# Kernel optimization log

Hardware: AMD Instinct MI355X
Metric: run time of the kernel (lower is better)

Reference implementation:

```python
import jax, jax.numpy as jnp
import numpy as np

NB, NC, IN, HID, OUT, ENG = 8, 16384, 64, 128, 64, 128
SYNC, DEBATE = 0.15, 0.15


def setup_inputs() -> dict:
    key = jax.random.key(0)
    ks = jax.random.split(key, 24)
    rn = lambda k, s, sc=0.05: jax.random.normal(k, s, jnp.float32) * sc
    return {
        "x": jax.random.normal(ks[0], (1, IN), jnp.float32),
        "noise": jax.random.normal(ks[1], (NB, 1, IN), jnp.float32),
        "amps": jax.random.uniform(ks[2], (NB,), jnp.float32, 0.5, 1.5),
        "hiddens": jax.random.normal(ks[3], (NB, NC, HID), jnp.float32) * 0.1,
        "eaW1": rn(ks[4], (ENG, IN + HID)), "eaB1": rn(ks[5], (ENG,)),
        "eaW2": rn(ks[6], (OUT, ENG)), "eaB2": rn(ks[7], (OUT,)),
        "egW1": rn(ks[8], (ENG, IN + HID)), "egB1": rn(ks[9], (ENG,)),
        "egW2": rn(ks[10], (OUT, ENG)), "egB2": rn(ks[11], (OUT,)),
        "gru_Wih": rn(ks[12], (3 * HID, OUT + 1)), "gru_Whh": rn(ks[13], (3 * HID, HID)),
        "gru_bih": rn(ks[14], (3 * HID,)), "gru_bhh": rn(ks[15], (3 * HID,)),
        "headW": rn(ks[16], (IN, OUT)), "headb": rn(ks[17], (IN,)),
        "mixW": rn(ks[18], (HID, HID * NB)), "mixb": rn(ks[19], (HID,)),
        "step": 10,
    }


def reference(x, noise, amps, hiddens, eaW1, eaB1, eaW2, eaB2,
              egW1, egB1, egW2, egB2, gru_Wih, gru_Whh, gru_bih, gru_bhh,
              headW, headb, mixW, mixb, step):
    sg = jax.lax.stop_gradient
    # per-branch perturbed input, broadcast over cells
    scale = 0.05 * jnp.arange(1, NB + 1, dtype=x.dtype)[:, None, None]
    xb = jnp.broadcast_to(x[None] + noise * scale, (NB, NC, IN))
    comb = jnp.concatenate([xb, hiddens], axis=-1)          # (NB,NC,IN+HID)
    a = jax.nn.relu(comb @ eaW1.T + eaB1) @ eaW2.T + eaB2
    g = jax.nn.relu(comb @ egW1.T + egB1) @ egW2.T + egB2
    out = a - g                                             # (NB,NC,OUT)
    tension = jnp.mean(out ** 2, axis=-1)                   # (NB,NC)

    # GRUCell update (mem input is detached in the original)
    mem_in = sg(jnp.concatenate([out, tension[..., None]], axis=-1))
    gi = mem_in @ gru_Wih.T + gru_bih                       # (NB,NC,3H)
    gh = hiddens @ gru_Whh.T + gru_bhh
    ir, iz, inn = jnp.split(gi, 3, axis=-1)
    hr, hz, hn = jnp.split(gh, 3, axis=-1)
    r = jax.nn.sigmoid(ir + hr)
    z = jax.nn.sigmoid(iz + hz)
    n = jnp.tanh(inn + r * hn)
    newh = sg((1.0 - z) * n + z * hiddens)                  # stored detached

    # faction sync + debate (state only)
    nf = min(8, NC // 2)
    fs = NC // nf
    core = newh[:, :nf * fs].reshape(NB, nf, fs, HID)
    core = (1.0 - SYNC) * core + SYNC * core.mean(axis=2, keepdims=True)
    if step > 5:
        glob = core.mean(axis=2).mean(axis=1)               # (NB,HID)
        dc = max(1, fs // 4)
        core = core.at[:, :, :dc].set(
            (1.0 - DEBATE) * core[:, :, :dc] + DEBATE * glob[:, None, None, :])
    newh = jnp.concatenate([core.reshape(NB, nf * fs, HID), newh[:, nf * fs:]], axis=1)

    # amplitude-weighted branch combine (amps used via .item() -> constants)
    aabs = jnp.abs(amps)
    aabs = aabs / (aabs.sum() + 1e-8)
    cell_out = jnp.einsum('b,bnd->nd', sg(aabs), out)       # (NC,OUT)
    avg_t = tension.mean(axis=0)                            # (NC,)
    w = jax.nn.softmax(sg(avg_t))                           # weights from .item()'d tensions
    combined = (w[:, None] * cell_out).sum(axis=0, keepdims=True)  # (1,OUT)
    pred = combined @ headW.T + headb                       # (1,IN)

    # interference mixer state update on branch 0
    interf = newh.mean(axis=1).reshape(1, -1) @ mixW.T + mixb       # (1,HID)
    newh = newh.at[0].add(sg(interf) * 0.05)

    return pred, avg_t.mean(), newh
```

## Files before the change

### kernel.cpp

```cpp
#include <hip/hip_runtime.h>
#include <math.h>

#define NB   8
#define NCC  16384
#define HID  128

typedef __attribute__((ext_vector_type(8))) short short8;
typedef __attribute__((ext_vector_type(4))) float f32x4;

#define MFMA(a,b,c) __builtin_amdgcn_mfma_f32_16x16x32_bf16(a,b,c,0,0,0)

#define WS_AABS   0
#define WS_BASE1  8
#define WS_BOUT   2056
#define WS_BSUMR  2120
#define WS_BSUMZ  2248
#define WS_BIHN   2376
#define WS_BHHN   2504
#define WS_W64    2632
#define WS_INTERF 3024
#define WS_FRAG   3152
#define WS_SD     64592
#define WS_AVGT   73808
#define WS_TS     90192
#define WS_FMEAN  221264
#define WS_PART2  230480
#define WS_FPART  246864
#define WS_CO     771152
#define WS_PARTE  1819728
#define WS_PARTA  1819984

__device__ __forceinline__ unsigned short f2b(float f) {
    unsigned int u = __float_as_uint(f);
    unsigned int r = (u + 0x7fffu + ((u >> 16) & 1u)) >> 16;
    return (unsigned short)r;
}
__device__ __forceinline__ float b2f(unsigned short us) {
    return __uint_as_float(((unsigned int)us) << 16);
}
__device__ __forceinline__ float sigm(float x) {
    return __builtin_amdgcn_rcpf(1.f + __expf(-x));
}
__device__ __forceinline__ float tanh_fast(float x) {
    return 1.f - 2.f * __builtin_amdgcn_rcpf(__expf(2.f * x) + 1.f);
}
__device__ __forceinline__ unsigned int cvtpk(float lo, float hi) {
    unsigned int r;
    asm volatile("v_cvt_pk_bf16_f32 %0, %1, %2" : "=v"(r) : "v"(lo), "v"(hi));
    return r;
}
__device__ __forceinline__ void stg(char* dst, int row, int cb, float4 u, float4 v) {
    uint4 pk = make_uint4(cvtpk(u.x, u.y), cvtpk(u.z, u.w),
                          cvtpk(v.x, v.y), cvtpk(v.z, v.w));
    *(uint4*)(dst + row * 256 + (cb ^ ((row & 7) << 4))) = pk;
}

__global__ __launch_bounds__(1024) void kprep(
    const float* __restrict__ x, const float* __restrict__ noise,
    const float* __restrict__ amps,
    const float* __restrict__ eaW1, const float* __restrict__ eaB1,
    const float* __restrict__ egW1, const float* __restrict__ egB1,
    const float* __restrict__ eaW2, const float* __restrict__ eaB2,
    const float* __restrict__ egW2, const float* __restrict__ egB2,
    const float* __restrict__ gWih, const float* __restrict__ gWhh,
    const float* __restrict__ gbih, const float* __restrict__ gbhh,
    float* __restrict__ ws)
{
    int i = blockIdx.x * 1024 + threadIdx.x;
    if (i < 122880) {
        short* wsh = (short*)(ws + WS_FRAG);
        float v;
        if (i < 32768) {
            int rel = i;
            int j = rel & 7, l = (rel >> 3) & 63, tk = rel >> 9;
            int kt = tk & 3, nt = tk >> 2;
            int n = nt * 16 + (l & 15), k = kt * 32 + ((l >> 4) << 3) + j;
            v = (n < 128) ? eaW1[n * 192 + 64 + k] : egW1[(n - 128) * 192 + 64 + k];
        } else if (i < 49152) {
            int rel = i - 32768;
            int j = rel & 7, l = (rel >> 3) & 63, tk = rel >> 9;
            int kt = tk & 7, nt = tk >> 3;
            int d = nt * 16 + (l & 15), k = kt * 32 + ((l >> 4) << 3) + j;
            v = (k < 128) ? eaW2[d * 128 + k] : -egW2[d * 128 + (k - 128)];
        } else if (i < 73728) {
            int rel = i - 49152;
            int j = rel & 7, l = (rel >> 3) & 63, tk = rel >> 9;
            int kt = tk & 1, nt = tk >> 1;
            int r = nt * 16 + (l & 15), k = kt * 32 + ((l >> 4) << 3) + j;
            v = gWih[r * 65 + k];
        } else {
            int rel = i - 73728;
            int j = rel & 7, l = (rel >> 3) & 63, tk = rel >> 9;
            int kt = tk & 3, nt = tk >> 2;
            int r = nt * 16 + (l & 15), k = kt * 32 + ((l >> 4) << 3) + j;
            v = gWhh[r * 128 + k];
        }
        wsh[i] = (short)f2b(v);
    }
    if (blockIdx.x == 0) {
        __shared__ float xb[8][64];
        int t = threadIdx.x;
        if (t < 512) {
            int b = t >> 6, k = t & 63;
            xb[b][k] = x[k] + noise[b * 64 + k] * (0.05f * (float)(b + 1));
        }
        if (t == 0) {
            float s = 0.f;
            for (int b = 0; b < 8; b++) s += fabsf(amps[b]);
            s += 1e-8f;
            for (int b = 0; b < 8; b++) ws[WS_AABS + b] = fabsf(amps[b]) / s;
        }
        __syncthreads();
        for (int ii = t; ii < 2048; ii += 1024) {
            int b = ii >> 8, n = ii & 255;
            const float* Wp; float s;
            if (n < 128) { Wp = eaW1 + n * 192; s = eaB1[n]; }
            else         { Wp = egW1 + (n - 128) * 192; s = egB1[n - 128]; }
            for (int k = 0; k < 64; k++) s += xb[b & 7][k] * Wp[k];
            ws[WS_BASE1 + ii] = s;
        }
        if (t < 64) ws[WS_BOUT + t] = eaB2[t] - egB2[t];
        if (t < 128) {
            ws[WS_BSUMR + t] = gbih[t] + gbhh[t];
            ws[WS_BSUMZ + t] = gbih[128 + t] + gbhh[128 + t];
            ws[WS_BIHN + t]  = gbih[256 + t];
            ws[WS_BHHN + t]  = gbhh[256 + t];
        }
        if (t < 384) ws[WS_W64 + t] = gWih[t * 65 + 64];
    }
}

__global__ __launch_bounds__(1024) void kA(
    const float* __restrict__ hiddens, float* __restrict__ newh,
    float* __restrict__ ws)
{
    __shared__ char  wlds[98304];
    __shared__ char  hsb[64 * 256];
    __shared__ char  agb[64 * 512];
    __shared__ float ts_s[64];
    __shared__ float tsum_s[64];

    const int t    = threadIdx.x;
    const int lane = t & 63;
    const int w    = t >> 6;
    const int rg   = w >> 2;
    const int nq   = w & 3;
    const int col  = lane & 15;
    const int kq   = lane >> 4;
    const int r0   = rg * 16;
    const int n0   = blockIdx.x * 64;

    {
        const float4* src = (const float4*)(ws + WS_FRAG);
        float4* dst = (float4*)wlds;
#pragma unroll
        for (int p = 0; p < 6; p++) dst[p * 1024 + t] = src[p * 1024 + t];
    }
    const short8* W1F = (const short8*)wlds;
    const short8* W2F = (const short8*)(wlds + 65536);

    const float bo = ws[WS_BOUT + nq * 16 + col];
    float co_reg[4];
#pragma unroll
    for (int i = 0; i < 4; i++) co_reg[i] = 0.f;
    if (t < 64) tsum_s[t] = 0.f;

    const int flat = t * 8;
    const int srow = flat >> 7;
    const int scb  = (flat & 127) * 2;

    {
        const float* hs = hiddens + (size_t)n0 * HID;
        float4 a0 = *(const float4*)(hs + flat);
        float4 a1 = *(const float4*)(hs + flat + 4);
        stg(hsb, srow, scb, a0, a1);
    }
    float4 pfa0, pfa1;
    unsigned short* outu = (unsigned short*)newh;

    for (int b = 0; b < NB; ++b) {
        __syncthreads();
        if (t < 64) {
            if (b > 0) {
                ws[WS_TS + (size_t)(b - 1) * NCC + n0 + t] = ts_s[t];
                tsum_s[t] += ts_s[t];
            }
            ts_s[t] = 0.f;
        }
        if (b < 7) {
            const float* hsn = hiddens + ((size_t)((b + 1) * NCC + n0)) * HID;
            pfa0 = *(const float4*)(hsn + flat);
            pfa1 = *(const float4*)(hsn + flat + 4);
        }

        {
            short8 aH[4];
#pragma unroll
            for (int ks = 0; ks < 4; ks++) {
                int row = r0 + col;
                aH[ks] = *(const short8*)(hsb + row * 256 +
                           ((ks * 64 + (kq << 4)) ^ ((row & 7) << 4)));
            }
#pragma unroll
            for (int nti = 0; nti < 4; nti++) {
                int nt = nq * 4 + nti;
                f32x4 ac = {0.f, 0.f, 0.f, 0.f};
#pragma unroll
                for (int kt = 0; kt < 4; kt++)
                    ac = MFMA(aH[kt], W1F[(nt * 4 + kt) * 64 + lane], ac);
                int n = nt * 16 + col;
                float bs = ws[WS_BASE1 + b * 256 + n];
#pragma unroll
                for (int j = 0; j < 4; j++) {
                    int row = r0 + (kq << 2) + j;
                    float v = fmaxf(ac[j] + bs, 0.f);
                    *(unsigned short*)(agb + row * 512 +
                        ((n * 2) ^ ((row & 7) << 4))) = f2b(v);
                }
            }
        }
        __syncthreads();

        if (b < 7) stg(hsb, srow, scb, pfa0, pfa1);

        {
            f32x4 ov = {0.f, 0.f, 0.f, 0.f};
#pragma unroll
            for (int kt = 0; kt < 8; kt++) {
                int kb = kt * 64 + (kq << 4);
                int ra = r0 + col;
                short8 a0 = *(const short8*)(agb + ra * 512 + (kb ^ ((ra & 7) << 4)));
                ov = MFMA(a0, W2F[(nq * 8 + kt) * 64 + lane], ov);
            }
            int d = nq * 16 + col;
            float aab = ws[WS_AABS + b];
#pragma unroll
            for (int j = 0; j < 4; j++) {
                int row = r0 + (kq << 2) + j;
                float v = ov[j] + bo;
                co_reg[j] += aab * v;
                outu[(size_t)(b * NCC + n0 + row) * 256 + 192 + d] = f2b(v);
                float sq = v * v;
                sq += __shfl_xor(sq, 1);
                sq += __shfl_xor(sq, 2);
                sq += __shfl_xor(sq, 4);
                sq += __shfl_xor(sq, 8);
                if (col == 0) atomicAdd(&ts_s[row], sq);
            }
        }
    }
    __syncthreads();
    if (t < 64) {
        ws[WS_TS + (size_t)7 * NCC + n0 + t] = ts_s[t];
        tsum_s[t] += ts_s[t];
        ws[WS_AVGT + n0 + t] = tsum_s[t] * (1.f / 512.f);
    }
    {
        int d = nq * 16 + col;
#pragma unroll
        for (int j = 0; j < 4; j++) {
            int row = r0 + (kq << 2) + j;
            ws[WS_CO + (size_t)(n0 + row) * 64 + d] = co_reg[j];
        }
    }
}

__global__ __launch_bounds__(1024) void kB(
    const float* __restrict__ hiddens, float* __restrict__ newh,
    float* __restrict__ ws)
{
    __shared__ char  wl[98304];
    __shared__ char  hsb[64 * 256];
    __shared__ char  otb[64 * 128];
    __shared__ float ts_s[64];
    __shared__ float fp2[2][128];

    const int t    = threadIdx.x;
    const int lane = t & 63;
    const int w    = t >> 6;
    const int rg   = w >> 3;
    const int hg   = w & 7;
    const int col  = lane & 15;
    const int kq   = lane >> 4;
    const int chunk = blockIdx.x;
    const int n0   = chunk * 64;

    {
        const float4* src = (const float4*)(ws + WS_FRAG) + 9216;
        float4* dst = (float4*)wl;
#pragma unroll
        for (int p = 0; p < 6; p++) dst[p * 1024 + t] = src[p * 1024 + t];
    }
    const short8* WHHF = (const short8*)wl;
    const unsigned short* outu = (const unsigned short*)newh;

    const short8* WIHG = (const short8*)((const short*)(ws + WS_FRAG) + 49152);
    short8 wihR[2], wihZ[2], wihI[2];
#pragma unroll
    for (int ks = 0; ks < 2; ks++) {
        wihR[ks] = WIHG[(hg * 2 + ks) * 64 + lane];
        wihZ[ks] = WIHG[((hg + 8) * 2 + ks) * 64 + lane];
        wihI[ks] = WIHG[((hg + 16) * 2 + ks) * 64 + lane];
    }

    const int h = hg * 16 + col;
    const float bsr = ws[WS_BSUMR + h];
    const float bsz = ws[WS_BSUMZ + h];
    const float bin = ws[WS_BIHN + h];
    const float bhn = ws[WS_BHHN + h];
    const float wr  = ws[WS_W64 + h];
    const float wz  = ws[WS_W64 + 128 + h];
    const float wn  = ws[WS_W64 + 256 + h];

    const int flat = t * 8;
    const int srow = flat >> 7;
    const int scb  = (flat & 127) * 2;
    const int ocell = t >> 4;
    const int ooff  = (t & 15) * 4;

    float4 rh0, rh1;
    uint2  ro;
    float  rts = 0.f;
    {
        const float* hs = hiddens + (size_t)n0 * HID;
        rh0 = *(const float4*)(hs + flat);
        rh1 = *(const float4*)(hs + flat + 4);
        ro  = *(const uint2*)(outu + (size_t)(n0 + ocell) * 256 + 192 + ooff);
    }
    if (t < 64) rts = ws[WS_TS + n0 + t];

    for (int b = 0; b < NB; ++b) {
        stg(hsb, srow, scb, rh0, rh1);
        *(uint2*)(otb + ocell * 128 + ((ooff * 2) ^ ((ocell & 7) << 4))) = ro;
        if (t < 64) ts_s[t] = rts;
        __syncthreads();

        if (b < 7) {
            const float* hsn = hiddens + ((size_t)((b + 1) * NCC + n0)) * HID;
            rh0 = *(const float4*)(hsn + flat);
            rh1 = *(const float4*)(hsn + flat + 4);
            ro  = *(const uint2*)(outu + (size_t)((b + 1) * NCC + n0 + ocell) * 256 + 192 + ooff);
            if (t < 64) rts = ws[WS_TS + (size_t)(b + 1) * NCC + n0 + t];
        }

        {
            float* nbase = newh + ((size_t)(b * NCC + n0)) * HID;
            float flsum = 0.f;
#pragma unroll
            for (int st = 0; st < 2; ++st) {
                const int rbase = rg * 32 + st * 16;
                const int ra = rbase + col;
                f32x4 R = {0.f,0.f,0.f,0.f};
                f32x4 Z = {0.f,0.f,0.f,0.f};
                f32x4 I = {0.f,0.f,0.f,0.f};
                f32x4 N = {0.f,0.f,0.f,0.f};
#pragma unroll
                for (int ks = 0; ks < 2; ks++) {
                    short8 a0 = *(const short8*)(otb + ra * 128 +
                                 ((ks * 64 + (kq << 4)) ^ ((ra & 7) << 4)));
                    R = MFMA(a0, wihR[ks], R);
                    Z = MFMA(a0, wihZ[ks], Z);
                    I = MFMA(a0, wihI[ks], I);
                }
#pragma unroll
                for (int ks = 0; ks < 4; ks++) {
                    short8 a0 = *(const short8*)(hsb + ra * 256 +
                                 ((ks * 64 + (kq << 4)) ^ ((ra & 7) << 4)));
                    R = MFMA(a0, WHHF[(hg * 4 + ks) * 64 + lane], R);
                    Z = MFMA(a0, WHHF[((hg + 8) * 4 + ks) * 64 + lane], Z);
                    N = MFMA(a0, WHHF[((hg + 16) * 4 + ks) * 64 + lane], N);
                }
#pragma unroll
                for (int j = 0; j < 4; j++) {
                    int row = rbase + (kq << 2) + j;
                    float tv = ts_s[row] * (1.f / 64.f);
                    float r  = sigm(R[j] + bsr + tv * wr);
                    float z  = sigm(Z[j] + bsz + tv * wz);
                    float hn = N[j] + bhn;
                    float nn = tanh_fast(I[j] + bin + tv * wn + r * hn);
                    float hold = b2f(*(const unsigned short*)(hsb + row * 256 +
                                     ((h * 2) ^ ((row & 7) << 4))));
                    float nh = (1.f - z) * nn + z * hold;
                    nbase[(size_t)row * HID + h] = nh;
                    flsum += nh;
                }
            }
            flsum += __shfl_xor(flsum, 16);
            flsum += __shfl_xor(flsum, 32);
            if (kq == 0) fp2[rg][h] = flsum;
        }
        __syncthreads();

        if (t < 128)
            ws[WS_FPART + ((size_t)(b * 256 + chunk)) * 128 + t] = fp2[0][t] + fp2[1][t];
    }
}

__global__ __launch_bounds__(256) void kfr(float* __restrict__ ws)
{
    int blk = blockIdx.x, t = threadIdx.x;
    if (blk < 256) {
        __shared__ float wexp[64];
        __shared__ float red[256];
        int n0 = blk * 64;
        float av = 0.f;
        if (t < 64) {
            av = ws[WS_AVGT + n0 + t];
            wexp[t] = __expf(av);
        }
        __syncthreads();
        int d = t & 63, q = t >> 6;
        float s = 0.f;
        for (int i = 0; i < 16; i++) {
            int c = q * 16 + i;
            s += wexp[c] * ws[WS_CO + (size_t)(n0 + c) * 64 + d];
        }
        red[t] = s; __syncthreads();
        if (t < 64)
            ws[WS_PART2 + blk * 64 + t] = red[t] + red[64 + t] + red[128 + t] + red[192 + t];
        if (t < 64) {
            float e = wexp[t], a2 = av;
            e  += __shfl_xor(e, 1);  a2 += __shfl_xor(a2, 1);
            e  += __shfl_xor(e, 2);  a2 += __shfl_xor(a2, 2);
            e  += __shfl_xor(e, 4);  a2 += __shfl_xor(a2, 4);
            e  += __shfl_xor(e, 8);  a2 += __shfl_xor(a2, 8);
            e  += __shfl_xor(e, 16); a2 += __shfl_xor(a2, 16);
            e  += __shfl_xor(e, 32); a2 += __shfl_xor(a2, 32);
            if (t == 0) { ws[WS_PARTE + blk] = e; ws[WS_PARTA + blk] = a2; }
        }
    } else {
        int bf = blk - 256;
        int b = bf >> 3, f = bf & 7;
        if (t < 128) {
            int h = t;
            float s = 0.f, s8 = 0.f;
            for (int j = 0; j < 32; j++) {
                float v = ws[WS_FPART + ((size_t)(b * 256 + f * 32 + j)) * 128 + h];
                s += v;
                if (j < 8) s8 += v;
            }
            ws[WS_FMEAN + (b * 8 + f) * 128 + h] = s * (1.f / 2048.f);
            ws[WS_SD + (b * 8 + f) * 128 + h] = s8;
        }
    }
}

__global__ __launch_bounds__(256) void kmp(
    const float* __restrict__ mixW, const float* __restrict__ mixb,
    const float* __restrict__ headW, const float* __restrict__ headb,
    const int* __restrict__ step, float* __restrict__ ws,
    float* __restrict__ d_out)
{
    int blk = blockIdx.x, t = threadIdx.x;
    if (blk < 128) {
        __shared__ float hm[1024];
        __shared__ float red[256];
        bool deb = (step[0] > 5);
        for (int j = t; j < 1024; j += 256) {
            int b = j >> 7, hh = j & 127;
            float s = 0.f, sd = 0.f;
            for (int f = 0; f < 8; f++) {
                s  += ws[WS_FMEAN + (b * 8 + f) * 128 + hh];
                sd += ws[WS_SD + (b * 8 + f) * 128 + hh];
            }
            float gl = s * 0.125f;
            float tot = 16384.f * gl;
            if (deb) tot += 0.15f * (3481.6f * gl - 0.85f * sd);
            hm[j] = tot * (1.f / 16384.f);
        }
        __syncthreads();
        float4 wv = *(const float4*)(mixW + (size_t)blk * 1024 + t * 4);
        float4 hv = *(const float4*)(&hm[t * 4]);
        float s = wv.x * hv.x + wv.y * hv.y + wv.z * hv.z + wv.w * hv.w;
        red[t] = s; __syncthreads();
        for (int st = 128; st > 0; st >>= 1) { if (t < st) red[t] += red[t + st]; __syncthreads(); }
        if (t == 0) ws[WS_INTERF + blk] = mixb[blk] + red[0];
    } else {
        __shared__ float red[256];
        __shared__ float num[64];
        __shared__ float den_s;
        int d = t & 63, q = t >> 6;
        float s = 0.f;
        for (int i = 0; i < 64; i++) s += ws[WS_PART2 + (q * 64 + i) * 64 + d];
        red[t] = s; __syncthreads();
        if (t < 64) num[t] = red[t] + red[64 + t] + red[128 + t] + red[192 + t];
        __syncthreads();
        red[t] = ws[WS_PARTE + t]; __syncthreads();
        for (int st = 128; st > 0; st >>= 1) { if (t < st) red[t] += red[t + st]; __syncthreads(); }
        if (t == 0) den_s = red[0];
        __syncthreads();
        red[t] = ws[WS_PARTA + t]; __syncthreads();
        for (int st = 128; st > 0; st >>= 1) { if (t < st) red[t] += red[t + st]; __syncthreads(); }
        if (t == 0) d_out[64] = red[0] * (1.f / (float)NCC);
        __syncthreads();
        if (t < 64) {
            float inv_den = 1.f / den_s;
            float p = headb[t];
            for (int d2 = 0; d2 < 64; d2++) p += (num[d2] * inv_den) * headW[t * 64 + d2];
            d_out[t] = p;
        }
    }
}

__global__ __launch_bounds__(256) void k35_blend(
    float* __restrict__ newh, const float* __restrict__ ws,
    const int* __restrict__ step)
{
    int blk = blockIdx.x;
    int b = blk >> 8, ck = blk & 255;
    int t = threadIdx.x;
    int h4 = t & 31;
    int cg = t >> 5;
    int base = ck * 64;
    int f = base >> 11;
    bool deb = (step[0] > 5) && ((base & 2047) < 512);
    float4 fm = *(const float4*)(ws + WS_FMEAN + (size_t)(b * 8 + f) * 128 + h4 * 4);
    float glx = 0.f, gly = 0.f, glz = 0.f, glw = 0.f;
    for (int ff = 0; ff < 8; ff++) {
        float4 v = *(const float4*)(ws + WS_FMEAN + (size_t)(b * 8 + ff) * 128 + h4 * 4);
        glx += v.x; gly += v.y; glz += v.z; glw += v.w;
    }
    glx *= 0.125f; gly *= 0.125f; glz *= 0.125f; glw *= 0.125f;
    float4 itf = {0.f, 0.f, 0.f, 0.f};
    if (b == 0) {
        float4 iv = *(const float4*)(ws + WS_INTERF + h4 * 4);
        itf.x = 0.05f * iv.x; itf.y = 0.05f * iv.y;
        itf.z = 0.05f * iv.z; itf.w = 0.05f * iv.w;
    }
    for (int i = 0; i < 8; i++) {
        int cell = base + i * 8 + cg;
        size_t idx = ((size_t)b * NCC + cell) * 128 + h4 * 4;
        float4 v = *(float4*)(newh + idx);
        v.x = 0.85f * v.x + 0.15f * fm.x;
        v.y = 0.85f * v.y + 0.15f * fm.y;
        v.z = 0.85f * v.z + 0.15f * fm.z;
        v.w = 0.85f * v.w + 0.15f * fm.w;
        if (deb) {
            v.x = 0.85f * v.x + 0.15f * glx;
            v.y = 0.85f * v.y + 0.15f * gly;
            v.z = 0.85f * v.z + 0.15f * glz;
            v.w = 0.85f * v.w + 0.15f * glw;
        }
        v.x += itf.x; v.y += itf.y; v.z += itf.z; v.w += itf.w;
        *(float4*)(newh + idx) = v;
    }
}

extern "C" void kernel_launch(void* const* d_in, const int* in_sizes, int n_in,
                              void* d_out, int out_size, void* d_ws, size_t ws_size,
                              hipStream_t stream)
{
    const float* x       = (const float*)d_in[0];
    const float* noise   = (const float*)d_in[1];
    const float* amps    = (const float*)d_in[2];
    const float* hiddens = (const float*)d_in[3];
    const float* eaW1    = (const float*)d_in[4];
    const float* eaB1    = (const float*)d_in[5];
    const float* eaW2    = (const float*)d_in[6];
    const float* eaB2    = (const float*)d_in[7];
    const float* egW1    = (const float*)d_in[8];
    const float* egB1    = (const float*)d_in[9];
    const float* egW2    = (const float*)d_in[10];
    const float* egB2    = (const float*)d_in[11];
    const float* gWih    = (const float*)d_in[12];
    const float* gWhh    = (const float*)d_in[13];
    const float* gbih    = (const float*)d_in[14];
    const float* gbhh    = (const float*)d_in[15];
    const float* headW   = (const float*)d_in[16];
    const float* headb   = (const float*)d_in[17];
    const float* mixW    = (const float*)d_in[18];
    const float* mixb    = (const float*)d_in[19];
    const int*   step    = (const int*)d_in[20];

    float* out  = (float*)d_out;
    float* newh = out + 65;
    float* ws   = (float*)d_ws;

    kprep<<<120, 1024, 0, stream>>>(x, noise, amps, eaW1, eaB1, egW1, egB1,
                                    eaW2, eaB2, egW2, egB2, gWih, gWhh,
                                    gbih, gbhh, ws);
    kA<<<256, 1024, 0, stream>>>(hiddens, newh, ws);
    kB<<<256, 1024, 0, stream>>>(hiddens, newh, ws);
    kfr<<<320, 256, 0, stream>>>(ws);
    kmp<<<129, 256, 0, stream>>>(mixW, mixb, headW, headb, step, ws, out);
    k35_blend<<<2048, 256, 0, stream>>>(newh, ws, step);
}
```

Baseline: 119.3 us.

## Split GRU kernel kB across hidden-dimension halves to double grid size

Kernel kB now launches 512 blocks instead of 256, with each block covering one half of the 128 hidden units for a 64-cell chunk. Each block loads only the W_hh fragments for its half, permuted into a compact LDS layout, so shared memory per block drops from 96KB to 48KB. Each wave now does one 16-row MFMA tile instead of two. The aim is more parallelism and possibly two resident blocks per CU. The cost is that every block still stages the full hidden and output tiles, so global reads of hiddens and out are duplicated. A redundant `b & 7` index in kprep is also simplified.

```diff
diff --git a/kernel.cpp b/kernel.cpp
--- a/kernel.cpp
+++ b/kernel.cpp
@@ -116,7 +116,7 @@
             const float* Wp; float s;
             if (n < 128) { Wp = eaW1 + n * 192; s = eaB1[n]; }
             else         { Wp = egW1 + (n - 128) * 192; s = egB1[n - 128]; }
-            for (int k = 0; k < 64; k++) s += xb[b & 7][k] * Wp[k];
+            for (int k = 0; k < 64; k++) s += xb[b][k] * Wp[k];
             ws[WS_BASE1 + ii] = s;
         }
         if (t < 64) ws[WS_BOUT + t] = eaB2[t] - egB2[t];
@@ -269,29 +269,38 @@
     const float* __restrict__ hiddens, float* __restrict__ newh,
     float* __restrict__ ws)
 {
-    __shared__ char  wl[98304];
+    __shared__ char  wl[49152];
     __shared__ char  hsb[64 * 256];
     __shared__ char  otb[64 * 128];
     __shared__ float ts_s[64];
-    __shared__ float fp2[2][128];
+    __shared__ float fp4[4][64];
 
     const int t    = threadIdx.x;
     const int lane = t & 63;
     const int w    = t >> 6;
-    const int rg   = w >> 3;
-    const int hg   = w & 7;
+    const int rg   = w >> 2;
+    const int hq   = w & 3;
     const int col  = lane & 15;
     const int kq   = lane >> 4;
-    const int chunk = blockIdx.x;
+    const int chunk = blockIdx.x & 255;
+    const int half  = blockIdx.x >> 8;
+    const int hg   = half * 4 + hq;
     const int n0   = chunk * 64;
 
     {
-        const float4* src = (const float4*)(ws + WS_FRAG) + 9216;
+        const float4* src = (const float4*)(ws + WS_FRAG);
         float4* dst = (float4*)wl;
 #pragma unroll
-        for (int p = 0; p < 6; p++) dst[p * 1024 + t] = src[p * 1024 + t];
-    }
-    const short8* WHHF = (const short8*)wl;
+        for (int p = 0; p < 3; p++) {
+            int i = p * 1024 + t;
+            int l = i >> 6, ln = i & 63;
+            int gate = l >> 4, rem = l & 15;
+            int nt = gate * 8 + half * 4 + (rem >> 2);
+            int ks = rem & 3;
+            dst[i] = src[9216 + (nt * 4 + ks) * 64 + ln];
+        }
+    }
+    const short8* WHHL = (const short8*)wl;
     const unsigned short* outu = (const unsigned short*)newh;
 
     const short8* WIHG = (const short8*)((const short*)(ws + WS_FRAG) + 49152);
@@ -345,54 +354,52 @@
 
         {
             float* nbase = newh + ((size_t)(b * NCC + n0)) * HID;
+            const int rbase = rg * 16;
+            const int ra = rbase + col;
+            f32x4 R = {0.f,0.f,0.f,0.f};
+            f32x4 Z = {0.f,0.f,0.f,0.f};
+            f32x4 I = {0.f,0.f,0.f,0.f};
+            f32x4 N = {0.f,0.f,0.f,0.f};
+#pragma unroll
+            for (int ks = 0; ks < 2; ks++) {
+                short8 a0 = *(const short8*)(otb + ra * 128 +
+                             ((ks * 64 + (kq << 4)) ^ ((ra & 7) << 4)));
+                R = MFMA(a0, wihR[ks], R);
+                Z = MFMA(a0, wihZ[ks], Z);
+                I = MFMA(a0, wihI[ks], I);
+            }
+#pragma unroll
+            for (int ks = 0; ks < 4; ks++) {
+                short8 a0 = *(const short8*)(hsb + ra * 256 +
+                             ((ks * 64 + (kq << 4)) ^ ((ra & 7) << 4)));
+                R = MFMA(a0, WHHL[(hq * 4 + ks) * 64 + lane], R);
+                Z = MFMA(a0, WHHL[((16 + hq * 4) + ks) * 64 + lane], Z);
+                N = MFMA(a0, WHHL[((32 + hq * 4) + ks) * 64 + lane], N);
+            }
             float flsum = 0.f;
 #pragma unroll
-            for (int st = 0; st < 2; ++st) {
-                const int rbase = rg * 32 + st * 16;
-                const int ra = rbase + col;
-                f32x4 R = {0.f,0.f,0.f,0.f};
-                f32x4 Z = {0.f,0.f,0.f,0.f};
-                f32x4 I = {0.f,0.f,0.f,0.f};
-                f32x4 N = {0.f,0.f,0.f,0.f};
-#pragma unroll
-                for (int ks = 0; ks < 2; ks++) {
-                    short8 a0 = *(const short8*)(otb + ra * 128 +
-                                 ((ks * 64 + (kq << 4)) ^ ((ra & 7) << 4)));
-                    R = MFMA(a0, wihR[ks], R);
-                    Z = MFMA(a0, wihZ[ks], Z);
-                    I = MFMA(a0, wihI[ks], I);
-                }
-#pragma unroll
-                for (int ks = 0; ks < 4; ks++) {
-                    short8 a0 = *(const short8*)(hsb + ra * 256 +
-                                 ((ks * 64 + (kq << 4)) ^ ((ra & 7) << 4)));
-                    R = MFMA(a0, WHHF[(hg * 4 + ks) * 64 + lane], R);
-                    Z = MFMA(a0, WHHF[((hg + 8) * 4 + ks) * 64 + lane], Z);
-                    N = MFMA(a0, WHHF[((hg + 16) * 4 + ks) * 64 + lane], N);
-                }
-#pragma unroll
-                for (int j = 0; j < 4; j++) {
-                    int row = rbase + (kq << 2) + j;
-                    float tv = ts_s[row] * (1.f / 64.f);
-                    float r  = sigm(R[j] + bsr + tv * wr);
-                    float z  = sigm(Z[j] + bsz + tv * wz);
-                    float hn = N[j] + bhn;
-                    float nn = tanh_fast(I[j] + bin + tv * wn + r * hn);
-                    float hold = b2f(*(const unsigned short*)(hsb + row * 256 +
-                                     ((h * 2) ^ ((row & 7) << 4))));
-                    float nh = (1.f - z) * nn + z * hold;
-                    nbase[(size_t)row * HID + h] = nh;
-                    flsum += nh;
-                }
+            for (int j = 0; j < 4; j++) {
+                int row = rbase + (kq << 2) + j;
+                float tv = ts_s[row] * (1.f / 64.f);
+                float r  = sigm(R[j] + bsr + tv * wr);
+                float z  = sigm(Z[j] + bsz + tv * wz);
+                float hn = N[j] + bhn;
+                float nn = tanh_fast(I[j] + bin + tv * wn + r * hn);
+                float hold = b2f(*(const unsigned short*)(hsb + row * 256 +
+                                 ((h * 2) ^ ((row & 7) << 4))));
+                float nh = (1.f - z) * nn + z * hold;
+                nbase[(size_t)row * HID + h] = nh;
+                flsum += nh;
             }
             flsum += __shfl_xor(flsum, 16);
             flsum += __shfl_xor(flsum, 32);
-            if (kq == 0) fp2[rg][h] = flsum;
-        }
-        __syncthreads();
-
-        if (t < 128)
-            ws[WS_FPART + ((size_t)(b * 256 + chunk)) * 128 + t] = fp2[0][t] + fp2[1][t];
+            if (kq == 0) fp4[rg][hq * 16 + col] = flsum;
+        }
+        __syncthreads();
+
+        if (t < 64)
+            ws[WS_FPART + ((size_t)(b * 256 + chunk)) * 128 + half * 64 + t] =
+                fp4[0][t] + fp4[1][t] + fp4[2][t] + fp4[3][t];
     }
 }
 
@@ -580,7 +587,7 @@
                                     eaW2, eaB2, egW2, egB2, gWih, gWhh,
                                     gbih, gbhh, ws);
     kA<<<256, 1024, 0, stream>>>(hiddens, newh, ws);
-    kB<<<256, 1024, 0, stream>>>(hiddens, newh, ws);
+    kB<<<512, 1024, 0, stream>>>(hiddens, newh, ws);
     kfr<<<320, 256, 0, stream>>>(ws);
     kmp<<<129, 256, 0, stream>>>(mixW, mixb, headW, headb, step, ws, out);
     k35_blend<<<2048, 256, 0, stream>>>(newh, ws, step);
```

After: 129.1 us. 8.2% more time.

## Double-buffer kB shared staging and drop per-branch reduction barrier

Applied to the files above, without the earlier changes.

The GRU kernel now keeps two shared-memory copies of the hidden, output and tension tiles. The next branch's tile is written into the idle buffer after the current compute, so only one barrier per branch iteration is needed instead of two. The per-row-group column sums are written straight to the workspace, doubling that partial-sum area, and the reduction kernel now adds the two halves itself. This costs about 25 KB more shared memory per block and more workspace traffic, and it relies on the workspace partial-sum region being large enough for the wider layout.

```diff
diff --git a/kernel.cpp b/kernel.cpp
--- a/kernel.cpp
+++ b/kernel.cpp
@@ -116,7 +116,7 @@
             const float* Wp; float s;
             if (n < 128) { Wp = eaW1 + n * 192; s = eaB1[n]; }
             else         { Wp = egW1 + (n - 128) * 192; s = egB1[n - 128]; }
-            for (int k = 0; k < 64; k++) s += xb[b & 7][k] * Wp[k];
+            for (int k = 0; k < 64; k++) s += xb[b][k] * Wp[k];
             ws[WS_BASE1 + ii] = s;
         }
         if (t < 64) ws[WS_BOUT + t] = eaB2[t] - egB2[t];
@@ -270,10 +270,9 @@
     float* __restrict__ ws)
 {
     __shared__ char  wl[98304];
-    __shared__ char  hsb[64 * 256];
-    __shared__ char  otb[64 * 128];
-    __shared__ float ts_s[64];
-    __shared__ float fp2[2][128];
+    __shared__ char  hsb[2][64 * 256];
+    __shared__ char  otb[2][64 * 128];
+    __shared__ float ts_s[2][64];
 
     const int t    = threadIdx.x;
     const int lane = t & 63;
@@ -318,23 +317,23 @@
     const int ocell = t >> 4;
     const int ooff  = (t & 15) * 4;
 
-    float4 rh0, rh1;
-    uint2  ro;
-    float  rts = 0.f;
     {
         const float* hs = hiddens + (size_t)n0 * HID;
-        rh0 = *(const float4*)(hs + flat);
-        rh1 = *(const float4*)(hs + flat + 4);
-        ro  = *(const uint2*)(outu + (size_t)(n0 + ocell) * 256 + 192 + ooff);
-    }
-    if (t < 64) rts = ws[WS_TS + n0 + t];
+        float4 a0 = *(const float4*)(hs + flat);
+        float4 a1 = *(const float4*)(hs + flat + 4);
+        uint2  o0 = *(const uint2*)(outu + (size_t)(n0 + ocell) * 256 + 192 + ooff);
+        stg(hsb[0], srow, scb, a0, a1);
+        *(uint2*)(otb[0] + ocell * 128 + ((ooff * 2) ^ ((ocell & 7) << 4))) = o0;
+        if (t < 64) ts_s[0][t] = ws[WS_TS + n0 + t];
+    }
 
     for (int b = 0; b < NB; ++b) {
-        stg(hsb, srow, scb, rh0, rh1);
-        *(uint2*)(otb + ocell * 128 + ((ooff * 2) ^ ((ocell & 7) << 4))) = ro;
-        if (t < 64) ts_s[t] = rts;
-        __syncthreads();
-
+        __syncthreads();
+        const int cur = b & 1;
+
+        float4 rh0, rh1;
+        uint2  ro;
+        float  rts = 0.f;
         if (b < 7) {
             const float* hsn = hiddens + ((size_t)((b + 1) * NCC + n0)) * HID;
             rh0 = *(const float4*)(hsn + flat);
@@ -356,7 +355,7 @@
                 f32x4 N = {0.f,0.f,0.f,0.f};
 #pragma unroll
                 for (int ks = 0; ks < 2; ks++) {
-                    short8 a0 = *(const short8*)(otb + ra * 128 +
+                    short8 a0 = *(const short8*)(otb[cur] + ra * 128 +
                                  ((ks * 64 + (kq << 4)) ^ ((ra & 7) << 4)));
                     R = MFMA(a0, wihR[ks], R);
                     Z = MFMA(a0, wihZ[ks], Z);
@@ -364,7 +363,7 @@
                 }
 #pragma unroll
                 for (int ks = 0; ks < 4; ks++) {
-                    short8 a0 = *(const short8*)(hsb + ra * 256 +
+                    short8 a0 = *(const short8*)(hsb[cur] + ra * 256 +
                                  ((ks * 64 + (kq << 4)) ^ ((ra & 7) << 4)));
                     R = MFMA(a0, WHHF[(hg * 4 + ks) * 64 + lane], R);
                     Z = MFMA(a0, WHHF[((hg + 8) * 4 + ks) * 64 + lane], Z);
@@ -373,12 +372,12 @@
 #pragma unroll
                 for (int j = 0; j < 4; j++) {
                     int row = rbase + (kq << 2) + j;
-                    float tv = ts_s[row] * (1.f / 64.f);
+                    float tv = ts_s[cur][row] * (1.f / 64.f);
                     float r  = sigm(R[j] + bsr + tv * wr);
                     float z  = sigm(Z[j] + bsz + tv * wz);
                     float hn = N[j] + bhn;
                     float nn = tanh_fast(I[j] + bin + tv * wn + r * hn);
-                    float hold = b2f(*(const unsigned short*)(hsb + row * 256 +
+                    float hold = b2f(*(const unsigned short*)(hsb[cur] + row * 256 +
                                      ((h * 2) ^ ((row & 7) << 4))));
                     float nh = (1.f - z) * nn + z * hold;
                     nbase[(size_t)row * HID + h] = nh;
@@ -387,12 +386,15 @@
             }
             flsum += __shfl_xor(flsum, 16);
             flsum += __shfl_xor(flsum, 32);
-            if (kq == 0) fp2[rg][h] = flsum;
-        }
-        __syncthreads();
-
-        if (t < 128)
-            ws[WS_FPART + ((size_t)(b * 256 + chunk)) * 128 + t] = fp2[0][t] + fp2[1][t];
+            if (kq == 0)
+                ws[WS_FPART + ((size_t)(b * 256 + chunk)) * 256 + rg * 128 + h] = flsum;
+        }
+
+        if (b < 7) {
+            stg(hsb[cur ^ 1], srow, scb, rh0, rh1);
+            *(uint2*)(otb[cur ^ 1] + ocell * 128 + ((ooff * 2) ^ ((ocell & 7) << 4))) = ro;
+            if (t < 64) ts_s[cur ^ 1][t] = rts;
+        }
     }
 }
 
@@ -435,7 +437,8 @@
             int h = t;
             float s = 0.f, s8 = 0.f;
             for (int j = 0; j < 32; j++) {
-                float v = ws[WS_FPART + ((size_t)(b * 256 + f * 32 + j)) * 128 + h];
+                size_t base = ((size_t)(b * 256 + f * 32 + j)) * 256;
+                float v = ws[WS_FPART + base + h] + ws[WS_FPART + base + 128 + h];
                 s += v;
                 if (j < 8) s8 += v;
             }
```

Result: slower. 128.1 us (+7.5%).
